# Performance work log

Hardware: AMD Instinct MI355X
Metric: run time of the kernel (lower is better)

The kernel has to match this reference:

```python
import jax, jax.numpy as jnp
import numpy as np

H = 1024
NUM_HEADS = 16
E = 4
I = H * 4 // E  # expert intermediate size = 1024
EPS = 1e-6


def layer_norm(x, g, b):
    mu = jnp.mean(x, axis=-1, keepdims=True)
    var = jnp.mean(jnp.square(x - mu), axis=-1, keepdims=True)
    return (x - mu) * jax.lax.rsqrt(var + EPS) * g + b


def setup_inputs() -> dict:
    key = jax.random.key(0)
    ks = jax.random.split(key, 12)
    B, Nq, Nkv = 4, 1024, 2048
    inp = {
        "query": jax.random.normal(ks[0], (B, Nq, H), jnp.float32),
        "key_value": jax.random.normal(ks[1], (B, Nkv, H), jnp.float32),
        "Wq": jax.random.normal(ks[2], (H, H), jnp.float32) * 0.02,
        "bq": jnp.zeros((H,), jnp.float32),
        "Wk": jax.random.normal(ks[3], (H, H), jnp.float32) * 0.02,
        "bk": jnp.zeros((H,), jnp.float32),
        "Wv": jax.random.normal(ks[4], (H, H), jnp.float32) * 0.02,
        "bv": jnp.zeros((H,), jnp.float32),
        "Wo": jax.random.normal(ks[5], (H, H), jnp.float32) * 0.02,
        "bo": jnp.zeros((H,), jnp.float32),
        "g1": jnp.ones((H,), jnp.float32),
        "b1": jnp.zeros((H,), jnp.float32),
        "g2": jnp.ones((H,), jnp.float32),
        "b2": jnp.zeros((H,), jnp.float32),
        "gate_up": jax.random.normal(ks[6], (E, H, 2 * I), jnp.float32) * 0.02,
        "down": jax.random.normal(ks[7], (E, I, H), jnp.float32) * 0.02,
    }
    return inp


def reference(query, key_value, Wq, bq, Wk, bk, Wv, bv, Wo, bo,
              g1, b1, g2, b2, gate_up, down):
    B, Nq, _ = query.shape
    Nkv = key_value.shape[1]
    d = H // NUM_HEADS
    scale = d ** -0.5

    # ---- cross-attention with pre-norm + residual ----
    x = layer_norm(query, g1, b1)
    q = (x @ Wq + bq).reshape(B, Nq, NUM_HEADS, d)
    k = (key_value @ Wk + bk).reshape(B, Nkv, NUM_HEADS, d)
    v = (key_value @ Wv + bv).reshape(B, Nkv, NUM_HEADS, d)
    scores = jnp.einsum("bqhd,bkhd->bhqk", q, k) * scale
    attn = jax.nn.softmax(scores, axis=-1)
    ctx = jnp.einsum("bhqk,bkhd->bqhd", attn, v).reshape(B, Nq, H)
    x = query + (ctx @ Wo + bo)

    # ---- token-routed MoE SwiGLU MLP (expert = pos % E) ----
    residual = x
    h = layer_norm(x, g2, b2)
    outs = []
    for e in range(E):
        xe = h[:, e::E]                      # [B, Nq/E, H] tokens routed to expert e
        gu = xe @ gate_up[e]                 # [B, Nq/E, 2I]
        gate, up = gu[..., :I], gu[..., I:]
        inter = jax.nn.silu(gate) * up
        outs.append(inter @ down[e])         # [B, Nq/E, H]
    moe = jnp.stack(outs, axis=2).reshape(B, Nq, H)  # interleave back to position order
    return residual + moe
```

## Files before the change

kernel.cpp:

```cpp
#include <hip/hip_runtime.h>
#include <hip/hip_bf16.h>

typedef unsigned short u16;
typedef float f32x4 __attribute__((ext_vector_type(4)));
typedef short s16x8 __attribute__((ext_vector_type(8)));

__device__ __forceinline__ u16 f2b(float f) {
    union { float f; unsigned u; } c; c.f = f;
    unsigned r = c.u + 0x7fffu + ((c.u >> 16) & 1u);
    return (u16)(r >> 16);
}
__device__ __forceinline__ unsigned pkbf16(float a, float b) {
    union { __hip_bfloat162 h; unsigned u; } c;
    c.h = __float22bfloat162_rn(float2{a, b});
    return c.u;
}

#define ASYNC_COPY16(gp, lp)                                                       \
    __builtin_amdgcn_global_load_lds(                                              \
        (const __attribute__((address_space(1))) void*)(gp),                       \
        (__attribute__((address_space(3))) void*)(lp), 16, 0, 0)

__device__ __forceinline__ void transcast_body(const float* __restrict__ Wz,
                                               u16* __restrict__ Wtz,
                                               int K, int N, int bx, int by,
                                               int permute) {
    __shared__ float tile[64][65];
    const int n0 = bx * 64, k0 = by * 64;
    const int tid = threadIdx.x;
    const int tx = tid & 15, ty = tid >> 4;
#pragma unroll
    for (int it = 0; it < 4; it++) {
        int r = ty + it * 16;
        float4 v = *(const float4*)&Wz[(size_t)(k0 + r) * N + n0 + tx * 4];
        tile[r][tx * 4 + 0] = v.x;
        tile[r][tx * 4 + 1] = v.y;
        tile[r][tx * 4 + 2] = v.z;
        tile[r][tx * 4 + 3] = v.w;
    }
    __syncthreads();
    int n = tid >> 2;
    int ks = (tid & 3) * 16;
    int drow = n0 + n;
    if (permute) drow = (drow < 1024) ? 2 * drow : 2 * (drow - 1024) + 1;
    u16* dst = &Wtz[(size_t)drow * K + k0 + ks];
#pragma unroll
    for (int h = 0; h < 2; h++) {
        uint4 o;
        o.x = pkbf16(tile[ks + h * 8 + 0][n], tile[ks + h * 8 + 1][n]);
        o.y = pkbf16(tile[ks + h * 8 + 2][n], tile[ks + h * 8 + 3][n]);
        o.z = pkbf16(tile[ks + h * 8 + 4][n], tile[ks + h * 8 + 5][n]);
        o.w = pkbf16(tile[ks + h * 8 + 6][n], tile[ks + h * 8 + 7][n]);
        *(uint4*)(dst + h * 8) = o;
    }
}

__device__ __forceinline__ void cast_body(const float* __restrict__ x,
                                          u16* __restrict__ y, int blk) {
    int id = blk * 256 + threadIdx.x;
    const float* p = x + (size_t)id * 8;
    float4 a = *(const float4*)p;
    float4 b = *(const float4*)(p + 4);
    uint4 o;
    o.x = pkbf16(a.x, a.y);
    o.y = pkbf16(a.z, a.w);
    o.z = pkbf16(b.x, b.y);
    o.w = pkbf16(b.z, b.w);
    *(uint4*)(y + (size_t)id * 8) = o;
}

__device__ __forceinline__ void ln_body(const float* __restrict__ x,
                                        const float* __restrict__ g,
                                        const float* __restrict__ bb,
                                        u16* __restrict__ out, int token, int pack) {
    int tid = threadIdx.x;
    const float* row = x + (size_t)token * 1024;
    float4 v = *(const float4*)(row + tid * 4);
    float s1 = v.x + v.y + v.z + v.w;
    float s2 = v.x * v.x + v.y * v.y + v.z * v.z + v.w * v.w;
#pragma unroll
    for (int off = 32; off > 0; off >>= 1) {
        s1 += __shfl_down(s1, off);
        s2 += __shfl_down(s2, off);
    }
    __shared__ float ws1[4], ws2[4];
    int wave = tid >> 6;
    if ((tid & 63) == 0) { ws1[wave] = s1; ws2[wave] = s2; }
    __syncthreads();
    float t1 = ws1[0] + ws1[1] + ws1[2] + ws1[3];
    float t2 = ws2[0] + ws2[1] + ws2[2] + ws2[3];
    float mean = t1 * (1.f / 1024.f);
    float var = t2 * (1.f / 1024.f) - mean * mean;
    float rstd = rsqrtf(var + 1e-6f);
    size_t dest = token;
    if (pack) {
        int bq = token >> 10, q = token & 1023;
        dest = (size_t)(q & 3) * 1024 + (size_t)bq * 256 + (q >> 2);
    }
    int c = tid * 4;
    float4 gv = *(const float4*)(g + c);
    float4 bv = *(const float4*)(bb + c);
    uint2 o;
    o.x = pkbf16((v.x - mean) * rstd * gv.x + bv.x, (v.y - mean) * rstd * gv.y + bv.y);
    o.y = pkbf16((v.z - mean) * rstd * gv.z + bv.z, (v.w - mean) * rstd * gv.w + bv.w);
    *(uint2*)&out[dest * 1024 + c] = o;
}

__global__ __launch_bounds__(256) void ln_kernel(const float* __restrict__ x,
                                                 const float* __restrict__ g,
                                                 const float* __restrict__ bb,
                                                 u16* __restrict__ out, int pack) {
    ln_body(x, g, bb, out, blockIdx.x, pack);
}

__global__ __launch_bounds__(256) void prep_kernel(
    const float* __restrict__ Wq, const float* __restrict__ Wk,
    const float* __restrict__ Wv, const float* __restrict__ Wo,
    u16* __restrict__ wqt, u16* __restrict__ wkt,
    u16* __restrict__ wvt, u16* __restrict__ wot,
    const float* __restrict__ gate_up, u16* __restrict__ gut,
    const float* __restrict__ down, u16* __restrict__ dnt,
    const float* __restrict__ key_value, u16* __restrict__ kvbf,
    const float* __restrict__ query, const float* __restrict__ g1,
    const float* __restrict__ b1, u16* __restrict__ xn) {
    const int idx = blockIdx.x;
    if (idx < 1024) {
        int z = idx >> 8, r = idx & 255;
        const float* W = (z == 0) ? Wq : (z == 1) ? Wk : (z == 2) ? Wv : Wo;
        u16* O = (z == 0) ? wqt : (z == 1) ? wkt : (z == 2) ? wvt : wot;
        transcast_body(W, O, 1024, 1024, r >> 4, r & 15, 0);
    } else if (idx < 3072) {
        int t = idx - 1024, z = t >> 9, r = t & 511;
        transcast_body(gate_up + (size_t)z * 2097152, gut + (size_t)z * 2097152,
                       1024, 2048, r >> 4, r & 15, 1);
    } else if (idx < 4096) {
        int t = idx - 3072, z = t >> 8, r = t & 255;
        transcast_body(down + (size_t)z * 1048576, dnt + (size_t)z * 1048576,
                       1024, 1024, r >> 4, r & 15, 0);
    } else if (idx < 8192) {
        cast_body(key_value, kvbf, idx - 4096);
    } else {
        ln_body(query, g1, b1, xn, idx - 8192, 0);
    }
}

template <int BM>
__device__ __forceinline__ void gemm_body(
    u16* lds,
    const u16* __restrict__ Ab, const u16* __restrict__ Bb,
    const float* __restrict__ bias0, const float* __restrict__ bias1, int biasSplit,
    const float* __restrict__ resid,
    float* __restrict__ outF, u16* __restrict__ outH, u16* __restrict__ outH2,
    int N, int K, long long oStride, int z, int mode, float outScale,
    int m0, int n0) {
    constexpr int NJ = (BM == 128) ? 4 : 2;
    constexpr int HALF = BM * 64 + 128 * 64;
    const int tid = threadIdx.x;
    const int wave = tid >> 6, lane = tid & 63;
    const int wm = (BM == 128) ? (wave >> 1) * 64 : 0;
    const int wn = (BM == 128) ? (wave & 1) * 64 : wave * 32;
    const int quad = lane >> 4, l16 = lane & 15;
    f32x4 acc[4][NJ] = {};

    auto stage = [&](int k0, int buf) {
        u16* As = lds + buf * HALF;
        u16* Bs = As + BM * 64;
#pragma unroll
        for (int i = 0; i < BM / 32; i++) {
            int id = tid + i * 256;
            int row = id >> 3, c = id & 7;
            int srcseg = c ^ (row & 7);
            ASYNC_COPY16(&Ab[(size_t)(m0 + row) * K + k0 + srcseg * 8],
                         As + (size_t)(wave * 64 + i * 256) * 8);
        }
#pragma unroll
        for (int i = 0; i < 4; i++) {
            int id = tid + i * 256;
            int row = id >> 3, c = id & 7;
            int srcseg = c ^ (row & 7);
            ASYNC_COPY16(&Bb[(size_t)(n0 + row) * K + k0 + srcseg * 8],
                         Bs + (size_t)(wave * 64 + i * 256) * 8);
        }
    };

    stage(0, 0);
    int cur = 0;
    for (int k0 = 0; k0 < K; k0 += 64) {
        __syncthreads();
        if (k0 + 64 < K) stage(k0 + 64, cur ^ 1);
        const u16* As = lds + cur * HALF;
        const u16* Bs = As + BM * 64;
#pragma unroll
        for (int kk = 0; kk < 2; kk++) {
            s16x8 af[4], bfr[NJ];
#pragma unroll
            for (int i = 0; i < 4; i++) {
                int row = wm + i * 16 + l16;
                af[i] = *(const s16x8*)&As[row * 64 + ((kk * 4 + quad) ^ (row & 7)) * 8];
            }
#pragma unroll
            for (int j = 0; j < NJ; j++) {
                int row = wn + j * 16 + l16;
                bfr[j] = *(const s16x8*)&Bs[row * 64 + ((kk * 4 + quad) ^ (row & 7)) * 8];
            }
#pragma unroll
            for (int i = 0; i < 4; i++)
#pragma unroll
                for (int j = 0; j < NJ; j++)
                    acc[i][j] = __builtin_amdgcn_mfma_f32_16x16x32_bf16(af[i], bfr[j], acc[i][j], 0, 0, 0);
        }
        cur ^= 1;
    }
#pragma unroll
    for (int i = 0; i < 4; i++) {
#pragma unroll
        for (int j = 0; j < NJ; j++) {
            int col = n0 + wn + j * 16 + l16;
            float bv = 0.f;
            if (bias0) bv = (col < biasSplit) ? bias0[col] : bias1[col - biasSplit];
            if (mode == 3) {
                float vr[4];
#pragma unroll
                for (int r = 0; r < 4; r++) vr[r] = acc[i][j][r] + bv;
                int row0 = m0 + wm + i * 16 + quad * 4;
                if (col < 1024) {
#pragma unroll
                    for (int r = 0; r < 4; r++)
                        outH[(size_t)(row0 + r) * 1024 + col] = f2b(vr[r]);
                } else {
                    int bb2 = row0 >> 11, key = row0 & 2047;
                    int hh = (col - 1024) >> 6, d = (col - 1024) & 63;
                    int cc = key >> 6, kk = key & 63;
                    int kk4 = kk >> 4, q4 = (kk >> 2) & 3;
                    int seg = (((kk4 >> 1) << 2) | q4) ^ (d & 7);
                    int half = kk4 & 1;
                    uint2 dw;
                    dw.x = pkbf16(vr[0], vr[1]);
                    dw.y = pkbf16(vr[2], vr[3]);
                    *(uint2*)&outH2[((((size_t)bb2 * 16 + hh) * 32 + cc) * 64 + d) * 64
                                    + seg * 8 + half * 4] = dw;
                }
                continue;
            }
#pragma unroll
            for (int r = 0; r < 4; r++) {
                int row = m0 + wm + i * 16 + quad * 4 + r;
                float v = acc[i][j][r] + bv;
                if (mode == 2) {
                    float other = __shfl_xor(v, 1);
                    if (!(lane & 1)) {
                        float res = (v / (1.f + __expf(-v))) * other;
                        outH[(size_t)z * oStride + (size_t)row * (N >> 1) + (col >> 1)] = f2b(res);
                    }
                } else if (mode == 1) {
                    int bb2 = row >> 8, qi = row & 255;
                    size_t oidx = ((size_t)bb2 * 1024 + (size_t)z + 4 * (size_t)qi) * N + col;
                    outF[oidx] = v + resid[oidx];
                } else {
                    size_t oidx = (size_t)z * oStride + (size_t)row * N + col;
                    if (resid) v += resid[oidx];
                    if (outF) outF[oidx] = v;
                    else outH[oidx] = f2b(v * outScale);
                }
            }
        }
    }
}

template <int BM>
__global__ __launch_bounds__(256) void gemm_t(
    const u16* __restrict__ A, const u16* __restrict__ Bt,
    const float* __restrict__ bias0, const float* __restrict__ bias1, int biasSplit,
    const float* __restrict__ resid,
    float* __restrict__ outF, u16* __restrict__ outH, u16* __restrict__ outH2,
    int N, int K,
    long long aStride, long long bStride, long long oStride,
    int mode, float outScale) {
    extern __shared__ __align__(16) u16 ldsb[];
    const int z = blockIdx.z;
    gemm_body<BM>(ldsb,
                  A + (size_t)z * aStride, Bt + (size_t)z * bStride,
                  bias0, bias1, biasSplit, resid, outF, outH, outH2,
                  N, K, oStride, z, mode, outScale,
                  blockIdx.y * BM, blockIdx.x * 128);
}

__global__ __launch_bounds__(256) void gemm_qkv(
    const u16* __restrict__ xn, const u16* __restrict__ wqt,
    const float* __restrict__ bq,
    const u16* __restrict__ kvbf, const u16* __restrict__ kvw,
    const float* __restrict__ bk, const float* __restrict__ bv,
    u16* __restrict__ qb, u16* __restrict__ kvb, u16* __restrict__ vtb,
    float qscale) {
    extern __shared__ __align__(16) u16 ldsb[];
    const int bid = blockIdx.x;
    if (bid < 1024) {
        int xcd = bid & 7, slot = bid >> 3;
        int by = xcd * 8 + (slot >> 4), bx = slot & 15;
        gemm_body<128>(ldsb, kvbf, kvw,
                       bk, bv, 1024, nullptr, nullptr, kvb, vtb,
                       2048, 1024, 0, 0, 3, 1.f,
                       by * 128, bx * 128);
    } else {
        int t = bid - 1024;
        int xcd = t & 7, slot = t >> 3;
        int by = xcd * 8 + (slot >> 3), bx = slot & 7;
        gemm_body<64>(ldsb, xn, wqt,
                      bq, bq, 1 << 30, nullptr, nullptr, qb, nullptr,
                      1024, 1024, 0, 0, 0, qscale,
                      by * 64, bx * 128);
    }
}

__global__ __launch_bounds__(512, 4) void flash_attn(
    const u16* __restrict__ Q, const u16* __restrict__ Kb,
    const u16* __restrict__ VT, u16* __restrict__ O) {
    const int lidx = blockIdx.x;
    const int xcd = lidx & 7, slot = lidx >> 3;
    const int g = xcd + 8 * (slot >> 3);
    const int qt = slot & 7;
    const int b = g >> 4, h = g & 15;
    const int tid = threadIdx.x, wave = tid >> 6, lane = tid & 63;
    const int quad = lane >> 4, l16 = lane & 15;
    const int q0 = qt * 128 + wave * 16;

    __shared__ __align__(16) u16 Ks[2][64 * 64];
    __shared__ __align__(16) u16 Vs[2][64 * 64];

    const size_t qrow = ((size_t)b * 1024 + q0 + l16) * 1024 + (size_t)h * 64;
    s16x8 qf0 = *(const s16x8*)&Q[qrow + quad * 8];
    s16x8 qf1 = *(const s16x8*)&Q[qrow + 32 + quad * 8];

    f32x4 o[4] = {};
    float l = 0.f;

    const int l7 = l16 & 7;
    int koff[4][2], voff[2][4];
#pragma unroll
    for (int kt = 0; kt < 4; kt++) {
        koff[kt][0] = (kt * 16 + l16) * 8 + (quad ^ l7);
        koff[kt][1] = (kt * 16 + l16) * 8 + ((4 + quad) ^ l7);
    }
#pragma unroll
    for (int c2 = 0; c2 < 2; c2++)
#pragma unroll
        for (int dt = 0; dt < 4; dt++)
            voff[c2][dt] = (dt * 16 + l16) * 8 + ((c2 * 4 + quad) ^ l7);

    const int krow = tid >> 3;
    const int ksrcseg = (tid & 7) ^ (krow & 7);
    const u16* kSrc = Kb + ((size_t)b * 2048) * 1024 + (size_t)h * 64
                        + (size_t)krow * 1024 + ksrcseg * 8;
    const u16* vSrc = VT + ((size_t)(b * 16 + h) * 32) * 4096 + (size_t)tid * 8;
    u16* const kDst0 = &Ks[0][(size_t)(wave * 64) * 8];
    u16* const kDst1 = &Ks[1][(size_t)(wave * 64) * 8];
    u16* const vDst0 = &Vs[0][(size_t)(wave * 64) * 8];
    u16* const vDst1 = &Vs[1][(size_t)(wave * 64) * 8];

    ASYNC_COPY16(kSrc, kDst0);
    ASYNC_COPY16(vSrc, vDst0);
    kSrc += 64 * 1024; vSrc += 4096;

    for (int c = 0; c < 32; c++) {
        __syncthreads();
        if (c < 31) {
            if (c & 1) { ASYNC_COPY16(kSrc, kDst0); ASYNC_COPY16(vSrc, vDst0); }
            else       { ASYNC_COPY16(kSrc, kDst1); ASYNC_COPY16(vSrc, vDst1); }
            kSrc += 64 * 1024; vSrc += 4096;
        }
        const uint4* Kp = (const uint4*)((c & 1) ? &Ks[1][0] : &Ks[0][0]);
        const uint4* Vp = (const uint4*)((c & 1) ? &Vs[1][0] : &Vs[0][0]);

        f32x4 s[4];
#pragma unroll
        for (int kt = 0; kt < 4; kt++) {
            union { uint4 v; s16x8 f; } a0, a1;
            a0.v = Kp[koff[kt][0]];
            a1.v = Kp[koff[kt][1]];
            f32x4 acc = {};
            acc = __builtin_amdgcn_mfma_f32_16x16x32_bf16(a0.f, qf0, acc, 0, 0, 0);
            s[kt] = __builtin_amdgcn_mfma_f32_16x16x32_bf16(a1.f, qf1, acc, 0, 0, 0);
        }

        union { uint4 v; s16x8 f; } vf0[4];
#pragma unroll
        for (int dt = 0; dt < 4; dt++) vf0[dt].v = Vp[voff[0][dt]];

        uint2 dw[4];
        float rs = 0.f;
#pragma unroll
        for (int kt = 0; kt < 4; kt++) {
            float p0 = __builtin_amdgcn_exp2f(s[kt][0]);
            float p1 = __builtin_amdgcn_exp2f(s[kt][1]);
            float p2 = __builtin_amdgcn_exp2f(s[kt][2]);
            float p3 = __builtin_amdgcn_exp2f(s[kt][3]);
            rs += (p0 + p1) + (p2 + p3);
            dw[kt].x = pkbf16(p0, p1);
            dw[kt].y = pkbf16(p2, p3);
        }
        l += rs;

        union { uint4 v; s16x8 f; } pf0, pf1;
        pf0.v = uint4{dw[0].x, dw[0].y, dw[1].x, dw[1].y};
        pf1.v = uint4{dw[2].x, dw[2].y, dw[3].x, dw[3].y};
        union { uint4 v; s16x8 f; } vf1[4];
#pragma unroll
        for (int dt = 0; dt < 4; dt++) vf1[dt].v = Vp[voff[1][dt]];
#pragma unroll
        for (int dt = 0; dt < 4; dt++)
            o[dt] = __builtin_amdgcn_mfma_f32_16x16x32_bf16(vf0[dt].f, pf0.f, o[dt], 0, 0, 0);
#pragma unroll
        for (int dt = 0; dt < 4; dt++)
            o[dt] = __builtin_amdgcn_mfma_f32_16x16x32_bf16(vf1[dt].f, pf1.f, o[dt], 0, 0, 0);
    }

    l += __shfl_xor(l, 16);
    l += __shfl_xor(l, 32);
    float inv = 1.f / l;
#pragma unroll
    for (int dt = 0; dt < 4; dt++) {
        uint2 dw;
        dw.x = pkbf16(o[dt][0] * inv, o[dt][1] * inv);
        dw.y = pkbf16(o[dt][2] * inv, o[dt][3] * inv);
        *(uint2*)&O[qrow + dt * 16 + quad * 4] = dw;
    }
}

extern "C" void kernel_launch(void* const* d_in, const int* in_sizes, int n_in,
                              void* d_out, int out_size, void* d_ws, size_t ws_size,
                              hipStream_t stream) {
    (void)in_sizes; (void)n_in; (void)out_size; (void)ws_size;
    const float* query     = (const float*)d_in[0];
    const float* key_value = (const float*)d_in[1];
    const float* Wq = (const float*)d_in[2];
    const float* bq = (const float*)d_in[3];
    const float* Wk = (const float*)d_in[4];
    const float* bk = (const float*)d_in[5];
    const float* Wv = (const float*)d_in[6];
    const float* bv = (const float*)d_in[7];
    const float* Wo = (const float*)d_in[8];
    const float* bo = (const float*)d_in[9];
    const float* g1 = (const float*)d_in[10];
    const float* b1 = (const float*)d_in[11];
    const float* g2 = (const float*)d_in[12];
    const float* b2 = (const float*)d_in[13];
    const float* gate_up = (const float*)d_in[14];
    const float* down    = (const float*)d_in[15];
    float* out = (float*)d_out;

    char* wsb = (char*)d_ws;
    size_t off = 0;
    auto alloc = [&](size_t bytes) {
        char* p = wsb + off;
        off += (bytes + 255) & ~(size_t)255;
        return (void*)p;
    };
    u16* buf8a = (u16*)alloc((size_t)4096 * 1024 * 2);
    u16* qb    = (u16*)alloc((size_t)4096 * 1024 * 2);
    u16* kvb   = (u16*)alloc((size_t)8192 * 1024 * 2);
    u16* vtb   = (u16*)alloc((size_t)8192 * 1024 * 2);
    u16* kvbf  = (u16*)alloc((size_t)8192 * 1024 * 2);
    float* x2  = (float*)alloc((size_t)4096 * 1024 * 4);
    u16* wqt   = (u16*)alloc((size_t)1024 * 1024 * 2);
    u16* kvw   = (u16*)alloc((size_t)2048 * 1024 * 2);
    u16* wot   = (u16*)alloc((size_t)1024 * 1024 * 2);
    u16* gut   = (u16*)alloc((size_t)4 * 2048 * 1024 * 2);
    u16* dnt   = (u16*)alloc((size_t)4 * 1024 * 1024 * 2);
    u16* xn = buf8a; u16* ctx = buf8a; u16* hp = buf8a;
    u16* inter = kvbf;
    const int BIG = 1 << 30;
    const float QSCALE = 0.125f * 1.44269504f;

    prep_kernel<<<12288, 256, 0, stream>>>(
        Wq, Wk, Wv, Wo, wqt, kvw, kvw + (size_t)1024 * 1024, wot,
        gate_up, gut, down, dnt, key_value, kvbf, query, g1, b1, xn);
    gemm_qkv<<<1536, 256, 65536, stream>>>(xn, wqt, bq, kvbf, kvw, bk, bv,
                                           qb, kvb, vtb, QSCALE);
    flash_attn<<<512, 512, 0, stream>>>(qb, kvb, vtb, ctx);
    gemm_t<64><<<dim3(8, 64, 1), 256, 49152, stream>>>(ctx, wot, bo, bo, BIG,
        query, x2, nullptr, nullptr, 1024, 1024, 0, 0, 0, 0, 1.f);
    ln_kernel<<<4096, 256, 0, stream>>>(x2, g2, b2, hp, 1);
    gemm_t<64><<<dim3(16, 16, 4), 256, 49152, stream>>>(hp, gut, nullptr, nullptr, BIG,
        nullptr, nullptr, inter, nullptr, 2048, 1024,
        (long long)1024 * 1024, (long long)2048 * 1024, (long long)1024 * 1024, 2, 1.f);
    gemm_t<64><<<dim3(8, 16, 4), 256, 49152, stream>>>(inter, dnt, nullptr, nullptr, BIG,
        x2, out, nullptr, nullptr, 1024, 1024,
        (long long)1024 * 1024, (long long)1024 * 1024, 0, 1, 1.f);
}
```

Before: 349.8 us.

## Deepen flash-attention K/V prefetch to a four-stage async LDS ring

The flash attention kernel moves from a double buffer to a four-slot LDS ring for K and V tiles, prefetching three tiles ahead. It replaces __syncthreads with explicit s_waitcnt vmcnt counts plus s_barrier, so the wait covers only the oldest tile's loads. The aim is to hide global-load latency behind the MFMA work. In exchange, LDS per block doubles to 64KB, which may lower occupancy, and the vmcnt bookkeeping depends on the exact number of outstanding loads. The GEMM LDS index rewrites are equivalent cosmetic simplifications.

```diff
diff --git a/kernel.cpp b/kernel.cpp
--- a/kernel.cpp
+++ b/kernel.cpp
@@ -154,7 +154,7 @@
     int N, int K, long long oStride, int z, int mode, float outScale,
     int m0, int n0) {
     constexpr int NJ = (BM == 128) ? 4 : 2;
-    constexpr int HALF = BM * 64 + 128 * 64;
+    constexpr int HALF = (BM + 128) * 64;
     const int tid = threadIdx.x;
     const int wave = tid >> 6, lane = tid & 63;
     const int wm = (BM == 128) ? (wave >> 1) * 64 : 0;
@@ -171,7 +171,7 @@
             int row = id >> 3, c = id & 7;
             int srcseg = c ^ (row & 7);
             ASYNC_COPY16(&Ab[(size_t)(m0 + row) * K + k0 + srcseg * 8],
-                         As + (size_t)(wave * 64 + i * 256) * 8);
+                         As + (size_t)id * 8);
         }
 #pragma unroll
         for (int i = 0; i < 4; i++) {
@@ -179,7 +179,7 @@
             int row = id >> 3, c = id & 7;
             int srcseg = c ^ (row & 7);
             ASYNC_COPY16(&Bb[(size_t)(n0 + row) * K + k0 + srcseg * 8],
-                         Bs + (size_t)(wave * 64 + i * 256) * 8);
+                         Bs + (size_t)id * 8);
         }
     };
 
@@ -324,8 +324,8 @@
     const int quad = lane >> 4, l16 = lane & 15;
     const int q0 = qt * 128 + wave * 16;
 
-    __shared__ __align__(16) u16 Ks[2][64 * 64];
-    __shared__ __align__(16) u16 Vs[2][64 * 64];
+    __shared__ __align__(16) u16 Ks[4][64 * 64];
+    __shared__ __align__(16) u16 Vs[4][64 * 64];
 
     const size_t qrow = ((size_t)b * 1024 + q0 + l16) * 1024 + (size_t)h * 64;
     s16x8 qf0 = *(const s16x8*)&Q[qrow + quad * 8];
@@ -352,24 +352,27 @@
     const u16* kSrc = Kb + ((size_t)b * 2048) * 1024 + (size_t)h * 64
                         + (size_t)krow * 1024 + ksrcseg * 8;
     const u16* vSrc = VT + ((size_t)(b * 16 + h) * 32) * 4096 + (size_t)tid * 8;
-    u16* const kDst0 = &Ks[0][(size_t)(wave * 64) * 8];
-    u16* const kDst1 = &Ks[1][(size_t)(wave * 64) * 8];
-    u16* const vDst0 = &Vs[0][(size_t)(wave * 64) * 8];
-    u16* const vDst1 = &Vs[1][(size_t)(wave * 64) * 8];
-
-    ASYNC_COPY16(kSrc, kDst0);
-    ASYNC_COPY16(vSrc, vDst0);
-    kSrc += 64 * 1024; vSrc += 4096;
+    u16* const kDstW = &Ks[0][0] + wave * 512;
+    u16* const vDstW = &Vs[0][0] + wave * 512;
+
+    auto stg = [&](int buf) {
+        ASYNC_COPY16(kSrc, kDstW + buf * 4096);
+        ASYNC_COPY16(vSrc, vDstW + buf * 4096);
+        kSrc += 64 * 1024; vSrc += 4096;
+    };
+    stg(0); stg(1); stg(2);
 
     for (int c = 0; c < 32; c++) {
-        __syncthreads();
-        if (c < 31) {
-            if (c & 1) { ASYNC_COPY16(kSrc, kDst0); ASYNC_COPY16(vSrc, vDst0); }
-            else       { ASYNC_COPY16(kSrc, kDst1); ASYNC_COPY16(vSrc, vDst1); }
-            kSrc += 64 * 1024; vSrc += 4096;
-        }
-        const uint4* Kp = (const uint4*)((c & 1) ? &Ks[1][0] : &Ks[0][0]);
-        const uint4* Vp = (const uint4*)((c & 1) ? &Vs[1][0] : &Vs[0][0]);
+        if (c <= 29)
+            asm volatile("s_waitcnt vmcnt(4) lgkmcnt(0)\ns_barrier" ::: "memory");
+        else if (c == 30)
+            asm volatile("s_waitcnt vmcnt(2) lgkmcnt(0)\ns_barrier" ::: "memory");
+        else
+            asm volatile("s_waitcnt vmcnt(0) lgkmcnt(0)\ns_barrier" ::: "memory");
+        if (c < 29) stg((c + 3) & 3);
+
+        const uint4* Kp = (const uint4*)&Ks[c & 3][0];
+        const uint4* Vp = (const uint4*)&Vs[c & 3][0];
 
         f32x4 s[4];
 #pragma unroll
```

Result: slower. 367.4 us (+5.0%).
